# Kernel optimization log

Measured on AMD Instinct MI355X. Metric: run time of the kernel, lower is better.

Reference implementation:

```python
import jax, jax.numpy as jnp
import numpy as np
import math

NUM_HEADS = 16
D_MODEL = 1024
B, T = 1, 4096


def setup_inputs() -> dict:
    key = jax.random.key(0)
    kx, kq, kk, kv, ko = jax.random.split(key, 5)
    s = 1.0 / math.sqrt(D_MODEL)
    return {
        "x": jax.random.normal(kx, (B, T, D_MODEL), dtype=jnp.float32),
        "Wq": jax.random.normal(kq, (D_MODEL, D_MODEL), dtype=jnp.float32) * s,
        "Wk": jax.random.normal(kk, (D_MODEL, D_MODEL), dtype=jnp.float32) * s,
        "Wv": jax.random.normal(kv, (D_MODEL, D_MODEL), dtype=jnp.float32) * s,
        "Wo": jax.random.normal(ko, (D_MODEL, D_MODEL), dtype=jnp.float32) * s,
    }


def reference(x, Wq, Wk, Wv, Wo):
    # x: (B, T, D); weights stored torch-Linear style: y = x @ W.T
    Bx, Tx, D = x.shape
    H = NUM_HEADS
    dk = D // H
    q = (x @ Wq.T).reshape(Bx, Tx, H, dk)  # (B,T,H,dk)
    k = (x @ Wk.T).reshape(Bx, Tx, H, dk)
    v = (x @ Wv.T).reshape(Bx, Tx, H, dk)
    # scores: (B,H,T,T), scaled dot-product
    scores = jnp.einsum("bthd,bshd->bhts", q, k) / math.sqrt(dk)
    causal_mask = jnp.triu(jnp.ones((Tx, Tx), dtype=bool), k=1)  # True above diag
    scores = jnp.where(causal_mask, jnp.float32(-jnp.inf), scores).astype(jnp.float32)
    attn = jax.nn.softmax(scores, axis=-1)  # fp32 softmax, as in the torch module
    out = jnp.einsum("bhts,bshd->bthd", attn, v).reshape(Bx, Tx, D)
    return out @ Wo.T
```

## Files before the change

### kernel.cpp

```cpp
#include <hip/hip_runtime.h>
#include <hip/hip_bf16.h>
#include <math.h>

typedef __attribute__((ext_vector_type(8)))  __bf16 bf16x8;
typedef __attribute__((ext_vector_type(4)))  __bf16 bf16x4;
typedef __attribute__((ext_vector_type(4)))  float  f32x4;
typedef __attribute__((ext_vector_type(16))) float  f32x16;

static constexpr int T_SEQ = 4096;
static constexpr int DM    = 1024;
static constexpr int NH    = 16;
static constexpr int SPLIT_QB   = 34;
static constexpr int SPLIT_ROWS = T_SEQ - SPLIT_QB * 64;
static constexpr float QSCALE = 0.125f * 1.44269504088896340736f;

__device__ __forceinline__ void gload16(const void* g, void* l) {
    __builtin_amdgcn_global_load_lds(
        (const __attribute__((address_space(1))) unsigned int*)g,
        (__attribute__((address_space(3))) unsigned int*)l,
        16, 0, 0);
}

__device__ __forceinline__ unsigned cvtpk_bf16(float a, float b) {
    unsigned r;
    asm("v_cvt_pk_bf16_f32 %0, %1, %2" : "=v"(r) : "v"(a), "v"(b));
    return r;
}
__device__ __forceinline__ void permswap(unsigned& x, unsigned& y) {
    asm("v_permlane32_swap_b32 %0, %1" : "+v"(x), "+v"(y));
}
__device__ __forceinline__ float xhalf_max(float v) {
    union { float f; unsigned u; } a, b;
    a.f = v; b.f = v;
    asm volatile("" : "+v"(b.u));
    permswap(a.u, b.u);
    return fmaxf(a.f, b.f);
}
__device__ __forceinline__ float xhalf_sum(float v) {
    union { float f; unsigned u; } a, b;
    a.f = v; b.f = v;
    asm volatile("" : "+v"(b.u));
    permswap(a.u, b.u);
    return a.f + b.f;
}

__global__ __launch_bounds__(256)
void cvt_bf16(const float* __restrict__ in, __bf16* __restrict__ out, int n4) {
    int i = blockIdx.x * blockDim.x + threadIdx.x;
    if (i >= n4) return;
    float4 v = ((const float4*)in)[i];
    bf16x4 o;
    o[0] = (__bf16)v.x; o[1] = (__bf16)v.y; o[2] = (__bf16)v.z; o[3] = (__bf16)v.w;
    ((bf16x4*)out)[i] = o;
}

__global__ __launch_bounds__(256)
void cvt4_bf16(const float* __restrict__ a0, const float* __restrict__ a1,
               const float* __restrict__ a2, const float* __restrict__ a3,
               __bf16* __restrict__ o0, __bf16* __restrict__ o1,
               __bf16* __restrict__ o2, __bf16* __restrict__ o3, int n4) {
    int i = blockIdx.x * blockDim.x + threadIdx.x;
    if (i >= n4) return;
    const float* in = blockIdx.y == 0 ? a0 : blockIdx.y == 1 ? a1 : blockIdx.y == 2 ? a2 : a3;
    __bf16* out     = blockIdx.y == 0 ? o0 : blockIdx.y == 1 ? o1 : blockIdx.y == 2 ? o2 : o3;
    float4 v = ((const float4*)in)[i];
    bf16x4 o;
    o[0] = (__bf16)v.x; o[1] = (__bf16)v.y; o[2] = (__bf16)v.z; o[3] = (__bf16)v.w;
    ((bf16x4*)out)[i] = o;
}

template<bool OUT_BF16>
__device__ __forceinline__ void gemm_body(const __bf16* __restrict__ A,
                                          const __bf16* __restrict__ B,
                                          void* __restrict__ Cout,
                                          int N, int K, float scale,
                                          int bx, int by) {
    __shared__ __align__(16) __bf16 Al[128 * 64];
    __shared__ __align__(16) __bf16 Bl[128 * 64];
    const int tid  = threadIdx.x;
    const int lane = tid & 63;
    const int wid  = tid >> 6;
    const int wr   = wid >> 1, wc = wid & 1;
    const int m0   = by * 128, n0 = bx * 128;
    const int r    = lane & 15, g = lane >> 4;

    f32x4 acc[4][4];
    const f32x4 z4 = {0.f, 0.f, 0.f, 0.f};
    #pragma unroll
    for (int i = 0; i < 4; ++i)
        #pragma unroll
        for (int j = 0; j < 4; ++j) acc[i][j] = z4;

    for (int kt = 0; kt < K; kt += 64) {
        __syncthreads();
        #pragma unroll
        for (int p = 0; p < 4; ++p) {
            int u    = p * 256 + tid;
            int row  = u >> 3;
            int col8 = (u & 7) ^ (row & 7);
            gload16(A + (size_t)(m0 + row) * K + kt + col8 * 8,
                    (char*)Al + (p * 256 + wid * 64) * 16);
            gload16(B + (size_t)(n0 + row) * K + kt + col8 * 8,
                    (char*)Bl + (p * 256 + wid * 64) * 16);
        }
        __syncthreads();
        __builtin_amdgcn_s_setprio(1);
        #pragma unroll
        for (int kk = 0; kk < 2; ++kk) {
            bf16x8 af[4], bfr[4];
            #pragma unroll
            for (int mi = 0; mi < 4; ++mi)
                af[mi] = *(const bf16x8*)&Al[(wr * 64 + mi * 16 + r) * 64 + (((kk * 4 + g) ^ (r & 7)) * 8)];
            #pragma unroll
            for (int nj = 0; nj < 4; ++nj)
                bfr[nj] = *(const bf16x8*)&Bl[(wc * 64 + nj * 16 + r) * 64 + (((kk * 4 + g) ^ (r & 7)) * 8)];
            #pragma unroll
            for (int mi = 0; mi < 4; ++mi)
                #pragma unroll
                for (int nj = 0; nj < 4; ++nj)
                    acc[mi][nj] = __builtin_amdgcn_mfma_f32_16x16x32_bf16(af[mi], bfr[nj], acc[mi][nj], 0, 0, 0);
        }
        __builtin_amdgcn_s_setprio(0);
    }
    #pragma unroll
    for (int mi = 0; mi < 4; ++mi)
        #pragma unroll
        for (int nj = 0; nj < 4; ++nj)
            #pragma unroll
            for (int j = 0; j < 4; ++j) {
                int row = m0 + wr * 64 + mi * 16 + g * 4 + j;
                int col = n0 + wc * 64 + nj * 16 + r;
                float v = acc[mi][nj][j] * scale;
                if (OUT_BF16) ((__bf16*)Cout)[(size_t)row * N + col] = (__bf16)v;
                else          ((float*)Cout)[(size_t)row * N + col]  = v;
            }
}

__global__ __launch_bounds__(256)
void gemm_qkv(const __bf16* __restrict__ A,
              const __bf16* __restrict__ W0, const __bf16* __restrict__ W1,
              const __bf16* __restrict__ W2,
              __bf16* __restrict__ O0, __bf16* __restrict__ O1, __bf16* __restrict__ O2) {
    const int z = blockIdx.z;
    const __bf16* B = z == 0 ? W0 : (z == 1 ? W1 : W2);
    __bf16*       C = z == 0 ? O0 : (z == 1 ? O1 : O2);
    float scale = z == 0 ? QSCALE : 1.0f;
    gemm_body<true>(A, B, C, DM, DM, scale, blockIdx.x, blockIdx.y);
}

__global__ __launch_bounds__(256)
void gemm_out(const __bf16* __restrict__ A, const __bf16* __restrict__ B,
              float* __restrict__ C) {
    gemm_body<false>(A, B, C, DM, DM, 1.0f, blockIdx.x, blockIdx.y);
}

__global__ __launch_bounds__(256)
void vtrans(const __bf16* __restrict__ V, __bf16* __restrict__ Vt) {
    __shared__ __bf16 tl[64][72];
    const int tid = threadIdx.x;
    const int t0  = blockIdx.x * 64;
    const int h   = blockIdx.y;
    #pragma unroll
    for (int p = 0; p < 2; ++p) {
        int c = p * 256 + tid, row = c >> 3, col8 = c & 7;
        *(bf16x8*)&tl[row][col8 * 8] =
            *(const bf16x8*)(V + (size_t)(t0 + row) * DM + h * 64 + col8 * 8);
    }
    __syncthreads();
    #pragma unroll
    for (int p = 0; p < 2; ++p) {
        int c = p * 256 + tid, d = c >> 3, tc8 = c & 7;
        bf16x8 o;
        #pragma unroll
        for (int e = 0; e < 8; ++e) o[e] = tl[tc8 * 8 + e][d];
        *(bf16x8*)(Vt + (size_t)(h * 64 + d) * T_SEQ + t0 + tc8 * 8) = o;
    }
}

__global__ __launch_bounds__(128)
void attn_fwd(const __bf16* __restrict__ Q, const __bf16* __restrict__ Kp,
              const __bf16* __restrict__ Vt, __bf16* __restrict__ O,
              __bf16* __restrict__ U, float* __restrict__ Ml)
{
    __shared__ __align__(16) __bf16 Kl[2][64 * 64];
    __shared__ __align__(16) __bf16 Vl[2][64 * 64];
    const int tid  = threadIdx.x;
    const int lane = tid & 63, wid = tid >> 6;
    const int l31  = lane & 31;
    const int hi   = lane >> 5;
    const int h    = blockIdx.x;
    const int y    = blockIdx.y;
    int qb, t0i, t1i, chunk;
    bool split;
    if (y < SPLIT_QB) {
        qb = (SPLIT_QB - 1) - y; t0i = 0; t1i = qb; split = false; chunk = 0;
    } else {
        int s = y - SPLIT_QB;
        qb = 63 - (s >> 1);
        int n = qb + 1, c0 = n - (n >> 1);
        split = true;
        if ((s & 1) == 0) { chunk = 0; t0i = 0;  t1i = c0 - 1; }
        else              { chunk = 1; t0i = c0; t1i = qb;     }
    }
    const int qw = qb * 64 + wid * 32;
    const int qg = qw + l31;

    bf16x8 qf[4];
    #pragma unroll
    for (int kd0 = 0; kd0 < 4; ++kd0)
        qf[kd0] = *(const bf16x8*)(Q + (size_t)qg * DM + h * 64 + kd0 * 16 + hi * 8);

    float m_i = -1e30f, l_i = 0.f;
    f32x16 oacc[2];
    #pragma unroll
    for (int d = 0; d < 2; ++d)
        #pragma unroll
        for (int e = 0; e < 16; ++e) oacc[d][e] = 0.f;

    auto stage_lds = [&](int t, int buf) {
        #pragma unroll
        for (int p = 0; p < 4; ++p) {
            int u    = p * 128 + tid;
            int row  = u >> 3;
            int col8 = (u & 7) ^ (row & 7);
            gload16(Kp + (size_t)(t * 64 + row) * DM + h * 64 + col8 * 8,
                    (char*)&Kl[buf][0] + (p * 128 + wid * 64) * 16);
            gload16(Vt + (size_t)(h * 64 + row) * T_SEQ + t * 64 + col8 * 8,
                    (char*)&Vl[buf][0] + (p * 128 + wid * 64) * 16);
        }
    };
    stage_lds(t0i, 0);
    if (t1i > t0i) stage_lds(t0i + 1, 1);
    __syncthreads();

    auto qk = [&](f32x16* sdst, int buf) {
        #pragma unroll
        for (int ksub = 0; ksub < 2; ++ksub) {
            const int row = ksub * 32 + l31;
            f32x16 a;
            #pragma unroll
            for (int e = 0; e < 16; ++e) a[e] = 0.f;
            #pragma unroll
            for (int kd0 = 0; kd0 < 4; ++kd0) {
                bf16x8 kf = *(const bf16x8*)
                    &Kl[buf][(row << 6) + ((((kd0 << 1) + hi) ^ (row & 7)) << 3)];
                a = __builtin_amdgcn_mfma_f32_32x32x16_bf16(kf, qf[kd0], a, 0, 0, 0);
            }
            sdst[ksub] = a;
        }
    };
    auto mask_sf = [&](f32x16* s, int t) {
        const int kb = (t << 6) + 4 * hi;
        #pragma unroll
        for (int ksub = 0; ksub < 2; ++ksub)
            #pragma unroll
            for (int e = 0; e < 16; ++e) {
                int k = kb + ksub * 32 + ((e & 3) + 8 * (e >> 2));
                if (k > qg) s[ksub][e] = -1e30f;
            }
    };

    f32x16 sf[2], sfn[2];
    qk(sf, 0);
    if (t0i == qb) mask_sf(sf, t0i);

    bf16x8 kreg[4], vreg[4];
    for (int t = t0i; t <= t1i; ++t) {
        const int cur = (t - t0i) & 1;
        const bool have_next  = (t + 1 <= t1i);
        const bool have_next2 = (t + 2 <= t1i);
        if (have_next2) {
            const int t2 = t + 2;
            #pragma unroll
            for (int p = 0; p < 4; ++p) {
                int u   = p * 128 + tid;
                int row = u >> 3;
                int c   = u & 7;
                kreg[p] = *(const bf16x8*)(Kp + (size_t)(t2 * 64 + row) * DM + h * 64 + c * 8);
                vreg[p] = *(const bf16x8*)(Vt + (size_t)(h * 64 + row) * T_SEQ + t2 * 64 + c * 8);
            }
        }
        __builtin_amdgcn_s_setprio(1);
        if (have_next) {
            qk(sfn, cur ^ 1);
            if (t + 1 == qb) mask_sf(sfn, t + 1);
        }
        __builtin_amdgcn_s_setprio(0);
        float pm;
        {
            float t0[8];
            #pragma unroll
            for (int e = 0; e < 8; ++e)
                t0[e] = fmaxf(fmaxf(sf[0][e], sf[0][e + 8]), fmaxf(sf[1][e], sf[1][e + 8]));
            #pragma unroll
            for (int s = 4; s > 0; s >>= 1)
                #pragma unroll
                for (int e = 0; e < s; ++e) t0[e] = fmaxf(t0[e], t0[e + s]);
            pm = xhalf_max(t0[0]);
        }
        if (pm > m_i + 8.f) {
            float al = exp2f(m_i - pm);
            m_i = pm;
            l_i *= al;
            #pragma unroll
            for (int d = 0; d < 2; ++d)
                #pragma unroll
                for (int e = 0; e < 16; ++e) oacc[d][e] *= al;
        }
        float p[32];
        #pragma unroll
        for (int i = 0; i < 32; ++i)
            p[i] = exp2f(sf[i >> 4][i & 15] - m_i);
        {
            float s0[8];
            #pragma unroll
            for (int e = 0; e < 8; ++e)
                s0[e] = (p[e] + p[e + 8]) + (p[e + 16] + p[e + 24]);
            #pragma unroll
            for (int s = 4; s > 0; s >>= 1)
                #pragma unroll
                for (int e = 0; e < s; ++e) s0[e] += s0[e + s];
            l_i += xhalf_sum(s0[0]);
        }
        __builtin_amdgcn_s_setprio(1);
        #pragma unroll
        for (int ks = 0; ks < 4; ++ks) {
            unsigned w0 = cvtpk_bf16(p[8 * ks + 0], p[8 * ks + 1]);
            unsigned w1 = cvtpk_bf16(p[8 * ks + 2], p[8 * ks + 3]);
            unsigned w2 = cvtpk_bf16(p[8 * ks + 4], p[8 * ks + 5]);
            unsigned w3 = cvtpk_bf16(p[8 * ks + 6], p[8 * ks + 7]);
            permswap(w0, w2);
            permswap(w1, w3);
            union { unsigned u[4]; bf16x8 v; } pu;
            pu.u[0] = w0; pu.u[1] = w1; pu.u[2] = w2; pu.u[3] = w3;
            #pragma unroll
            for (int dsub = 0; dsub < 2; ++dsub) {
                const int row = dsub * 32 + l31;
                bf16x8 vt = *(const bf16x8*)
                    &Vl[cur][(row << 6) + ((((ks << 1) + hi) ^ (row & 7)) << 3)];
                oacc[dsub] = __builtin_amdgcn_mfma_f32_32x32x16_bf16(vt, pu.v, oacc[dsub], 0, 0, 0);
            }
        }
        __builtin_amdgcn_s_setprio(0);
        if (have_next2) {
            __syncthreads();
            #pragma unroll
            for (int p = 0; p < 4; ++p) {
                int u   = p * 128 + tid;
                int row = u >> 3;
                int c   = u & 7;
                *(bf16x8*)&Kl[cur][(row << 6) + ((c ^ (row & 7)) << 3)] = kreg[p];
                *(bf16x8*)&Vl[cur][(row << 6) + ((c ^ (row & 7)) << 3)] = vreg[p];
            }
            __syncthreads();
        }
        if (have_next) {
            sf[0] = sfn[0];
            sf[1] = sfn[1];
        }
    }
    __syncthreads();
    __bf16* ow = &Kl[0][0] + wid * 2048;
    const float invl = split ? 1.0f : (1.f / l_i);
    #pragma unroll
    for (int dsub = 0; dsub < 2; ++dsub)
        #pragma unroll
        for (int e = 0; e < 16; ++e) {
            int d = dsub * 32 + ((e & 3) + 8 * (e >> 2)) + 4 * hi;
            float v = oacc[dsub][e] * invl;
            int bo = l31 * 128 + ((2 * d) ^ ((l31 & 7) << 4));
            *(__bf16*)((char*)ow + bo) = (__bf16)v;
        }
    if (!split) {
        #pragma unroll
        for (int i = 0; i < 4; ++i) {
            int u  = hi * 4 + i;
            int bo = l31 * 128 + ((u * 16) ^ ((l31 & 7) << 4));
            bf16x8 v8 = *(const bf16x8*)((char*)ow + bo);
            *(bf16x8*)(O + (size_t)qg * DM + h * 64 + u * 8) = v8;
        }
    } else {
        const int ridx = qg - SPLIT_QB * 64;
        #pragma unroll
        for (int i = 0; i < 4; ++i) {
            int u  = hi * 4 + i;
            int bo = l31 * 128 + ((u * 16) ^ ((l31 & 7) << 4));
            bf16x8 v8 = *(const bf16x8*)((char*)ow + bo);
            *(bf16x8*)(U + ((size_t)(chunk * NH + h) * SPLIT_ROWS + ridx) * 64 + u * 8) = v8;
        }
        if (hi == 0) {
            float* mlp = Ml + ((size_t)(chunk * NH + h) * SPLIT_ROWS + ridx) * 2;
            mlp[0] = m_i;
            mlp[1] = l_i;
        }
    }
}

__global__ __launch_bounds__(256)
void attn_combine(const __bf16* __restrict__ U, const float* __restrict__ Ml,
                  __bf16* __restrict__ O) {
    int gid = blockIdx.x * 256 + threadIdx.x;
    int rh  = gid >> 3;
    int e8  = gid & 7;
    int ridx = rh >> 4, h = rh & 15;
    const float* ml0 = Ml + ((size_t)(0 * NH + h) * SPLIT_ROWS + ridx) * 2;
    const float* ml1 = Ml + ((size_t)(1 * NH + h) * SPLIT_ROWS + ridx) * 2;
    float m0 = ml0[0], l0 = ml0[1], m1 = ml1[0], l1 = ml1[1];
    float M  = fmaxf(m0, m1);
    float s0 = exp2f(m0 - M), s1 = exp2f(m1 - M);
    float inv = 1.f / (l0 * s0 + l1 * s1);
    bf16x8 u0 = *(const bf16x8*)(U + ((size_t)(0 * NH + h) * SPLIT_ROWS + ridx) * 64 + e8 * 8);
    bf16x8 u1 = *(const bf16x8*)(U + ((size_t)(1 * NH + h) * SPLIT_ROWS + ridx) * 64 + e8 * 8);
    bf16x8 o;
    #pragma unroll
    for (int j = 0; j < 8; ++j)
        o[j] = (__bf16)(((float)u0[j] * s0 + (float)u1[j] * s1) * inv);
    *(bf16x8*)(O + (size_t)(SPLIT_QB * 64 + ridx) * DM + h * 64 + e8 * 8) = o;
}

extern "C" void kernel_launch(void* const* d_in, const int* in_sizes, int n_in,
                              void* d_out, int out_size, void* d_ws, size_t ws_size,
                              hipStream_t stream) {
    const float* x  = (const float*)d_in[0];
    const float* Wq = (const float*)d_in[1];
    const float* Wk = (const float*)d_in[2];
    const float* Wv = (const float*)d_in[3];
    const float* Wo = (const float*)d_in[4];
    float* out = (float*)d_out;

    char* ws = (char*)d_ws;
    const size_t MB = (size_t)1 << 20;
    __bf16* xb    = (__bf16*)(ws + 0 * MB);
    __bf16* VtG   = (__bf16*)(ws + 0 * MB);
    __bf16* wqb   = (__bf16*)(ws + 8 * MB);
    float*  MlB   = (float*)(ws + 8 * MB);
    __bf16* wkb   = (__bf16*)(ws + 10 * MB);
    __bf16* wvb   = (__bf16*)(ws + 12 * MB);
    __bf16* wob   = (__bf16*)(ws + 14 * MB);
    __bf16* Qb    = (__bf16*)(ws + 16 * MB);
    __bf16* Kb    = (__bf16*)(ws + 24 * MB);
    __bf16* Vb    = (__bf16*)(ws + 32 * MB);
    __bf16* UB    = (__bf16*)(ws + 32 * MB);
    __bf16* attnb = (__bf16*)(ws + 40 * MB);

    const int nX = T_SEQ * DM / 4;
    const int nW = DM * DM / 4;
    cvt_bf16<<<(nX + 255) / 256, 256, 0, stream>>>(x, xb, nX);
    cvt4_bf16<<<dim3((nW + 255) / 256, 4), 256, 0, stream>>>(Wq, Wk, Wv, Wo,
                                                             wqb, wkb, wvb, wob, nW);

    gemm_qkv<<<dim3(DM / 128, T_SEQ / 128, 3), 256, 0, stream>>>(xb, wqb, wkb, wvb, Qb, Kb, Vb);

    vtrans<<<dim3(T_SEQ / 64, NH), 256, 0, stream>>>(Vb, VtG);

    attn_fwd<<<dim3(NH, SPLIT_QB + 2 * (64 - SPLIT_QB)), 128, 0, stream>>>(
        Qb, Kb, VtG, attnb, UB, MlB);

    attn_combine<<<(SPLIT_ROWS * NH * 8) / 256, 256, 0, stream>>>(UB, MlB, attnb);

    gemm_out<<<dim3(DM / 128, T_SEQ / 128), 256, 0, stream>>>(attnb, wob, out);
}
```

Baseline: 165.2 us.

## Compute softmax row sums via MFMA with ones matrix, reorder split blocks first

Replaces the per-tile VALU reduction of softmax probabilities into l_i with an extra MFMA that multiplies a ones-row A operand by the bf16 P fragment, accumulating row sums in a matrix accumulator. It also reorders the grid so the split (long) query blocks are scheduled first, and uses three-input max for the row max reduction. This moves reduction work off the vector ALU onto the matrix core at the cost of one extra MFMA per k-step, extra accumulator registers, and row sums computed from bf16-rounded probabilities.

Result: slower. 205.9 us (+24.6%).

```diff
diff --git a/kernel.cpp b/kernel.cpp
--- a/kernel.cpp
+++ b/kernel.cpp
@@ -12,6 +12,7 @@
 static constexpr int NH    = 16;
 static constexpr int SPLIT_QB   = 34;
 static constexpr int SPLIT_ROWS = T_SEQ - SPLIT_QB * 64;
+static constexpr int NSPLIT_Y   = 2 * (64 - SPLIT_QB);
 static constexpr float QSCALE = 0.125f * 1.44269504088896340736f;
 
 __device__ __forceinline__ void gload16(const void* g, void* l) {
@@ -42,6 +43,9 @@
     asm volatile("" : "+v"(b.u));
     permswap(a.u, b.u);
     return a.f + b.f;
+}
+__device__ __forceinline__ float max3f(float a, float b, float c) {
+    return fmaxf(fmaxf(a, b), c);
 }
 
 __global__ __launch_bounds__(256)
@@ -192,15 +196,15 @@
     const int y    = blockIdx.y;
     int qb, t0i, t1i, chunk;
     bool split;
-    if (y < SPLIT_QB) {
-        qb = (SPLIT_QB - 1) - y; t0i = 0; t1i = qb; split = false; chunk = 0;
-    } else {
-        int s = y - SPLIT_QB;
-        qb = 63 - (s >> 1);
+    if (y < NSPLIT_Y) {
+        qb = 63 - (y >> 1);
         int n = qb + 1, c0 = n - (n >> 1);
         split = true;
-        if ((s & 1) == 0) { chunk = 0; t0i = 0;  t1i = c0 - 1; }
+        if ((y & 1) == 0) { chunk = 0; t0i = 0;  t1i = c0 - 1; }
         else              { chunk = 1; t0i = c0; t1i = qb;     }
+    } else {
+        qb = (SPLIT_QB - 1) - (y - NSPLIT_Y);
+        t0i = 0; t1i = qb; split = false; chunk = 0;
     }
     const int qw = qb * 64 + wid * 32;
     const int qg = qw + l31;
@@ -210,12 +214,21 @@
     for (int kd0 = 0; kd0 < 4; ++kd0)
         qf[kd0] = *(const bf16x8*)(Q + (size_t)qg * DM + h * 64 + kd0 * 16 + hi * 8);
 
-    float m_i = -1e30f, l_i = 0.f;
-    f32x16 oacc[2];
+    bf16x8 onesA;
+    {
+        __bf16 ov = (__bf16)((l31 == 0) ? 1.0f : 0.0f);
+        #pragma unroll
+        for (int e = 0; e < 8; ++e) onesA[e] = ov;
+    }
+
+    float m_i = -1e30f;
+    f32x16 oacc[2], lacc;
     #pragma unroll
     for (int d = 0; d < 2; ++d)
         #pragma unroll
         for (int e = 0; e < 16; ++e) oacc[d][e] = 0.f;
+    #pragma unroll
+    for (int e = 0; e < 16; ++e) lacc[e] = 0.f;
 
     auto stage_lds = [&](int t, int buf) {
         #pragma unroll
@@ -288,20 +301,19 @@
         __builtin_amdgcn_s_setprio(0);
         float pm;
         {
-            float t0[8];
+            float t8[8];
             #pragma unroll
             for (int e = 0; e < 8; ++e)
-                t0[e] = fmaxf(fmaxf(sf[0][e], sf[0][e + 8]), fmaxf(sf[1][e], sf[1][e + 8]));
-            #pragma unroll
-            for (int s = 4; s > 0; s >>= 1)
-                #pragma unroll
-                for (int e = 0; e < s; ++e) t0[e] = fmaxf(t0[e], t0[e + s]);
-            pm = xhalf_max(t0[0]);
+                t8[e] = fmaxf(max3f(sf[0][e], sf[0][e + 8], sf[1][e]), sf[1][e + 8]);
+            float u0 = max3f(t8[0], t8[1], t8[2]);
+            float u1 = max3f(t8[3], t8[4], t8[5]);
+            float u2 = max3f(t8[6], t8[7], u0);
+            pm = xhalf_max(fmaxf(u1, u2));
         }
         if (pm > m_i + 8.f) {
             float al = exp2f(m_i - pm);
             m_i = pm;
-            l_i *= al;
+            lacc[0] *= al;
             #pragma unroll
             for (int d = 0; d < 2; ++d)
                 #pragma unroll
@@ -311,17 +323,6 @@
         #pragma unroll
         for (int i = 0; i < 32; ++i)
             p[i] = exp2f(sf[i >> 4][i & 15] - m_i);
-        {
-            float s0[8];
-            #pragma unroll
-            for (int e = 0; e < 8; ++e)
-                s0[e] = (p[e] + p[e + 8]) + (p[e + 16] + p[e + 24]);
-            #pragma unroll
-            for (int s = 4; s > 0; s >>= 1)
-                #pragma unroll
-                for (int e = 0; e < s; ++e) s0[e] += s0[e + s];
-            l_i += xhalf_sum(s0[0]);
-        }
         __builtin_amdgcn_s_setprio(1);
         #pragma unroll
         for (int ks = 0; ks < 4; ++ks) {
@@ -340,6 +341,7 @@
                     &Vl[cur][(row << 6) + ((((ks << 1) + hi) ^ (row & 7)) << 3)];
                 oacc[dsub] = __builtin_amdgcn_mfma_f32_32x32x16_bf16(vt, pu.v, oacc[dsub], 0, 0, 0);
             }
+            lacc = __builtin_amdgcn_mfma_f32_32x32x16_bf16(onesA, pu.v, lacc, 0, 0, 0);
         }
         __builtin_amdgcn_s_setprio(0);
         if (have_next2) {
@@ -359,9 +361,10 @@
             sf[1] = sfn[1];
         }
     }
+    const float l_v = xhalf_sum(lacc[0]);
     __syncthreads();
     __bf16* ow = &Kl[0][0] + wid * 2048;
-    const float invl = split ? 1.0f : (1.f / l_i);
+    const float invl = split ? 1.0f : (1.f / l_v);
     #pragma unroll
     for (int dsub = 0; dsub < 2; ++dsub)
         #pragma unroll
@@ -391,7 +394,7 @@
         if (hi == 0) {
             float* mlp = Ml + ((size_t)(chunk * NH + h) * SPLIT_ROWS + ridx) * 2;
             mlp[0] = m_i;
-            mlp[1] = l_i;
+            mlp[1] = l_v;
         }
     }
 }
@@ -453,7 +456,7 @@
 
     vtrans<<<dim3(T_SEQ / 64, NH), 256, 0, stream>>>(Vb, VtG);
 
-    attn_fwd<<<dim3(NH, SPLIT_QB + 2 * (64 - SPLIT_QB)), 128, 0, stream>>>(
+    attn_fwd<<<dim3(NH, NSPLIT_Y + SPLIT_QB), 128, 0, stream>>>(
         Qb, Kb, VtG, attnb, UB, MlB);
 
     attn_combine<<<(SPLIT_ROWS * NH * 8) / 256, 256, 0, stream>>>(UB, MlB, attnb);
```

## Split causal attention KV range into up to three chunks for load balance

Applied to the files above, without the earlier changes.

Replaces the two-way split of the heavy query blocks with a three-tier scheme. The last 20 query blocks are split into three KV chunks, the middle 22 into two, and the first 22 run unsplit, giving 126 y-blocks per head. The goal is to even out per-workgroup work under the causal mask and raise parallelism. The combine kernel now merges up to three partial results. The workspace buffers are reassigned, and the transposed V is moved to a separate region so it no longer aliases the partial outputs.

Measured after the change: 163.5 us. About the same (-1.1%).

```diff
diff --git a/kernel.cpp b/kernel.cpp
--- a/kernel.cpp
+++ b/kernel.cpp
@@ -10,8 +10,11 @@
 static constexpr int T_SEQ = 4096;
 static constexpr int DM    = 1024;
 static constexpr int NH    = 16;
-static constexpr int SPLIT_QB   = 34;
-static constexpr int SPLIT_ROWS = T_SEQ - SPLIT_QB * 64;
+static constexpr int C2_QB    = 22;
+static constexpr int C3_QB    = 44;
+static constexpr int SPL_ROWS = T_SEQ - C2_QB * 64;
+static constexpr int C3_ROWS  = T_SEQ - C3_QB * 64;
+static constexpr int NY = 126;
 static constexpr float QSCALE = 0.125f * 1.44269504088896340736f;
 
 __device__ __forceinline__ void gload16(const void* g, void* l) {
@@ -180,7 +183,8 @@
 __global__ __launch_bounds__(128)
 void attn_fwd(const __bf16* __restrict__ Q, const __bf16* __restrict__ Kp,
               const __bf16* __restrict__ Vt, __bf16* __restrict__ O,
-              __bf16* __restrict__ U, float* __restrict__ Ml)
+              __bf16* __restrict__ U0, __bf16* __restrict__ U1,
+              __bf16* __restrict__ U2, float* __restrict__ Ml)
 {
     __shared__ __align__(16) __bf16 Kl[2][64 * 64];
     __shared__ __align__(16) __bf16 Vl[2][64 * 64];
@@ -190,18 +194,14 @@
     const int hi   = lane >> 5;
     const int h    = blockIdx.x;
     const int y    = blockIdx.y;
-    int qb, t0i, t1i, chunk;
-    bool split;
-    if (y < SPLIT_QB) {
-        qb = (SPLIT_QB - 1) - y; t0i = 0; t1i = qb; split = false; chunk = 0;
-    } else {
-        int s = y - SPLIT_QB;
-        qb = 63 - (s >> 1);
-        int n = qb + 1, c0 = n - (n >> 1);
-        split = true;
-        if ((s & 1) == 0) { chunk = 0; t0i = 0;  t1i = c0 - 1; }
-        else              { chunk = 1; t0i = c0; t1i = qb;     }
-    }
+    int qb, chunk, nc;
+    if (y < 60)       { qb = 63 - y / 3;        chunk = y % 3;        nc = 3; }
+    else if (y < 104) { int s = y - 60; qb = 43 - s / 2; chunk = s % 2; nc = 2; }
+    else              { qb = 21 - (y - 104);    chunk = 0;            nc = 1; }
+    const int n    = qb + 1;
+    const int base = n / nc, rem = n % nc;
+    const int t0i  = chunk * base + (chunk < rem ? chunk : rem);
+    const int t1i  = t0i + base + (chunk < rem ? 1 : 0) - 1;
     const int qw = qb * 64 + wid * 32;
     const int qg = qw + l31;
 
@@ -361,7 +361,7 @@
     }
     __syncthreads();
     __bf16* ow = &Kl[0][0] + wid * 2048;
-    const float invl = split ? 1.0f : (1.f / l_i);
+    const float invl = (nc > 1) ? 1.0f : (1.f / l_i);
     #pragma unroll
     for (int dsub = 0; dsub < 2; ++dsub)
         #pragma unroll
@@ -371,7 +371,7 @@
             int bo = l31 * 128 + ((2 * d) ^ ((l31 & 7) << 4));
             *(__bf16*)((char*)ow + bo) = (__bf16)v;
         }
-    if (!split) {
+    if (nc == 1) {
         #pragma unroll
         for (int i = 0; i < 4; ++i) {
             int u  = hi * 4 + i;
@@ -380,16 +380,21 @@
             *(bf16x8*)(O + (size_t)qg * DM + h * 64 + u * 8) = v8;
         }
     } else {
-        const int ridx = qg - SPLIT_QB * 64;
+        __bf16* Uc = (chunk == 0) ? U0 : (chunk == 1) ? U1 : U2;
+        const int rows  = (chunk == 2) ? C3_ROWS : SPL_ROWS;
+        const int ridx  = qg - ((chunk == 2) ? C3_QB * 64 : C2_QB * 64);
         #pragma unroll
         for (int i = 0; i < 4; ++i) {
             int u  = hi * 4 + i;
             int bo = l31 * 128 + ((u * 16) ^ ((l31 & 7) << 4));
             bf16x8 v8 = *(const bf16x8*)((char*)ow + bo);
-            *(bf16x8*)(U + ((size_t)(chunk * NH + h) * SPLIT_ROWS + ridx) * 64 + u * 8) = v8;
+            *(bf16x8*)(Uc + ((size_t)h * rows + ridx) * 64 + u * 8) = v8;
         }
         if (hi == 0) {
-            float* mlp = Ml + ((size_t)(chunk * NH + h) * SPLIT_ROWS + ridx) * 2;
+            size_t off = (chunk == 0) ? ((size_t)h * SPL_ROWS + (qg - C2_QB * 64))
+                       : (chunk == 1) ? ((size_t)NH * SPL_ROWS + (size_t)h * SPL_ROWS + (qg - C2_QB * 64))
+                                      : ((size_t)2 * NH * SPL_ROWS + (size_t)h * C3_ROWS + (qg - C3_QB * 64));
+            float* mlp = Ml + off * 2;
             mlp[0] = m_i;
             mlp[1] = l_i;
         }
@@ -397,25 +402,42 @@
 }
 
 __global__ __launch_bounds__(256)
-void attn_combine(const __bf16* __restrict__ U, const float* __restrict__ Ml,
+void attn_combine(const __bf16* __restrict__ U0, const __bf16* __restrict__ U1,
+                  const __bf16* __restrict__ U2, const float* __restrict__ Ml,
                   __bf16* __restrict__ O) {
     int gid = blockIdx.x * 256 + threadIdx.x;
     int rh  = gid >> 3;
     int e8  = gid & 7;
     int ridx = rh >> 4, h = rh & 15;
-    const float* ml0 = Ml + ((size_t)(0 * NH + h) * SPLIT_ROWS + ridx) * 2;
-    const float* ml1 = Ml + ((size_t)(1 * NH + h) * SPLIT_ROWS + ridx) * 2;
+    int qg   = C2_QB * 64 + ridx;
+    bool has3 = (qg >= C3_QB * 64);
+    const float* ml0 = Ml + ((size_t)h * SPL_ROWS + ridx) * 2;
+    const float* ml1 = Ml + ((size_t)NH * SPL_ROWS + (size_t)h * SPL_ROWS + ridx) * 2;
     float m0 = ml0[0], l0 = ml0[1], m1 = ml1[0], l1 = ml1[1];
-    float M  = fmaxf(m0, m1);
+    float m2 = -1e30f, l2 = 0.f;
+    if (has3) {
+        const float* ml2 = Ml + ((size_t)2 * NH * SPL_ROWS
+                                 + (size_t)h * C3_ROWS + (qg - C3_QB * 64)) * 2;
+        m2 = ml2[0]; l2 = ml2[1];
+    }
+    float M  = fmaxf(fmaxf(m0, m1), m2);
     float s0 = exp2f(m0 - M), s1 = exp2f(m1 - M);
-    float inv = 1.f / (l0 * s0 + l1 * s1);
-    bf16x8 u0 = *(const bf16x8*)(U + ((size_t)(0 * NH + h) * SPLIT_ROWS + ridx) * 64 + e8 * 8);
-    bf16x8 u1 = *(const bf16x8*)(U + ((size_t)(1 * NH + h) * SPLIT_ROWS + ridx) * 64 + e8 * 8);
+    float s2 = has3 ? exp2f(m2 - M) : 0.f;
+    float inv = 1.f / (l0 * s0 + l1 * s1 + l2 * s2);
+    bf16x8 u0 = *(const bf16x8*)(U0 + ((size_t)h * SPL_ROWS + ridx) * 64 + e8 * 8);
+    bf16x8 u1 = *(const bf16x8*)(U1 + ((size_t)h * SPL_ROWS + ridx) * 64 + e8 * 8);
     bf16x8 o;
-    #pragma unroll
-    for (int j = 0; j < 8; ++j)
-        o[j] = (__bf16)(((float)u0[j] * s0 + (float)u1[j] * s1) * inv);
-    *(bf16x8*)(O + (size_t)(SPLIT_QB * 64 + ridx) * DM + h * 64 + e8 * 8) = o;
+    if (has3) {
+        bf16x8 u2 = *(const bf16x8*)(U2 + ((size_t)h * C3_ROWS + (qg - C3_QB * 64)) * 64 + e8 * 8);
+        #pragma unroll
+        for (int j = 0; j < 8; ++j)
+            o[j] = (__bf16)((((float)u0[j] * s0 + (float)u1[j] * s1) + (float)u2[j] * s2) * inv);
+    } else {
+        #pragma unroll
+        for (int j = 0; j < 8; ++j)
+            o[j] = (__bf16)(((float)u0[j] * s0 + (float)u1[j] * s1) * inv);
+    }
+    *(bf16x8*)(O + (size_t)qg * DM + h * 64 + e8 * 8) = o;
 }
 
 extern "C" void kernel_launch(void* const* d_in, const int* in_sizes, int n_in,
@@ -431,17 +453,20 @@
     char* ws = (char*)d_ws;
     const size_t MB = (size_t)1 << 20;
     __bf16* xb    = (__bf16*)(ws + 0 * MB);
-    __bf16* VtG   = (__bf16*)(ws + 0 * MB);
+    __bf16* U0B   = (__bf16*)(ws + 0 * MB);
     __bf16* wqb   = (__bf16*)(ws + 8 * MB);
     float*  MlB   = (float*)(ws + 8 * MB);
     __bf16* wkb   = (__bf16*)(ws + 10 * MB);
+    __bf16* U2B   = (__bf16*)(ws + 10 * MB);
     __bf16* wvb   = (__bf16*)(ws + 12 * MB);
     __bf16* wob   = (__bf16*)(ws + 14 * MB);
     __bf16* Qb    = (__bf16*)(ws + 16 * MB);
     __bf16* Kb    = (__bf16*)(ws + 24 * MB);
     __bf16* Vb    = (__bf16*)(ws + 32 * MB);
-    __bf16* UB    = (__bf16*)(ws + 32 * MB);
+    __bf16* U1B   = (__bf16*)(ws + 32 * MB);
     __bf16* attnb = (__bf16*)(ws + 40 * MB);
+    __bf16* VtG   = (__bf16*)(ws + 0 * MB);
+    __bf16* VtR   = (__bf16*)(ws + 48 * MB);
 
     const int nX = T_SEQ * DM / 4;
     const int nW = DM * DM / 4;
@@ -451,12 +476,11 @@
 
     gemm_qkv<<<dim3(DM / 128, T_SEQ / 128, 3), 256, 0, stream>>>(xb, wqb, wkb, wvb, Qb, Kb, Vb);
 
-    vtrans<<<dim3(T_SEQ / 64, NH), 256, 0, stream>>>(Vb, VtG);
-
-    attn_fwd<<<dim3(NH, SPLIT_QB + 2 * (64 - SPLIT_QB)), 128, 0, stream>>>(
-        Qb, Kb, VtG, attnb, UB, MlB);
-
-    attn_combine<<<(SPLIT_ROWS * NH * 8) / 256, 256, 0, stream>>>(UB, MlB, attnb);
+    vtrans<<<dim3(T_SEQ / 64, NH), 256, 0, stream>>>(Vb, VtR);
+
+    attn_fwd<<<dim3(NH, NY), 128, 0, stream>>>(Qb, Kb, VtR, attnb, U0B, U1B, U2B, MlB);
+
+    attn_combine<<<(SPL_ROWS * NH * 8) / 256, 256, 0, stream>>>(U0B, U1B, U2B, MlB, attnb);
 
     gemm_out<<<dim3(DM / 128, T_SEQ / 128), 256, 0, stream>>>(attnb, wob, out);
 }
```
